# Kernel tuning notes

Hardware: AMD Instinct MI355X
Metric: run time of the kernel (lower is better)

The kernel has to match this reference:

```python
import jax, jax.numpy as jnp
import numpy as np

# 8-bit signed symmetric quantization grid (bit buffer in the module is set to 8 at runtime)
SAT_MAX = 127.0
SAT_MIN = -127.0


def _squant_stage(rn, re, un, ue, up_p, dn, de, dn_p):
    """One SQuant flip stage over the last axis (vectorized SQuant_func).

    For each row: e = sum(rounding_error); flip round(|e|) elements.
    If e < 0 (under-rounded overall) flip the highest-up-priority elements up,
    else flip the highest-down-priority elements down. The boundary (last,
    lowest-priority flipped) element gets a nonzero priority in the opposite
    direction so the next (coarser) stage can revert it — this reproduces the
    in-place priority update SQuant_func performs after zeroing priorities.
    All tensors have shape [..., K].
    """
    e_sum = jnp.sum(re, axis=-1)                                   # [...]
    n_flip = jnp.round(jnp.abs(e_sum)).astype(jnp.int32)[..., None]  # [...,1]
    flip_up = (e_sum < 0)[..., None]                               # [...,1]
    prio = jnp.where(flip_up, up_p, dn_p)
    order = jnp.argsort(-prio, axis=-1)        # descending priority
    rank = jnp.argsort(order, axis=-1)         # rank[i] = position of i in order
    mask = rank < n_flip                       # elements to flip
    rn2 = jnp.where(mask, jnp.where(flip_up, un, dn), rn)
    re2 = jnp.where(mask, jnp.where(flip_up, ue, de), re)
    # boundary element (rank == n_flip-1) gets opposite-direction priority
    boundary = mask & (rank == (n_flip - 1))
    b_prio = jnp.where(boundary, jnp.abs(re2), 0.0)
    up_p2 = jnp.where(flip_up, jnp.zeros_like(b_prio), b_prio)
    dn_p2 = jnp.where(flip_up, b_prio, jnp.zeros_like(b_prio))
    return rn2, re2, up_p2, dn_p2


def adaptive_round(x, t_min, t_max):
    rn = jnp.round(x)
    re = rn - x
    # up candidates: elements rounded down (re < 0) and not saturated high
    ue = jnp.where((x >= t_max) | (re > 0), 0.0, re)
    up_p = jnp.abs(ue)
    nz_u = ue != 0
    ue = jnp.where(nz_u, ue + 1.0, ue)
    un = jnp.where(nz_u, rn + 1.0, rn)
    # down candidates: elements rounded up (re > 0) and not saturated low
    de = jnp.where((x <= t_min) | (re < 0), 0.0, re)
    dn_p = jnp.abs(de)
    nz_d = de != 0
    de = jnp.where(nz_d, de - 1.0, de)
    dn = jnp.where(nz_d, rn - 1.0, rn)

    OC, IC = x.shape[0], x.shape[1]
    K = x.size // (OC * IC)
    shp_k = (OC, IC, K)         # squant-k: per (oc, ic) kernel row
    rn_k, re_k, up_p_k, dn_p_k = _squant_stage(
        rn.reshape(shp_k), re.reshape(shp_k),
        un.reshape(shp_k), ue.reshape(shp_k), up_p.reshape(shp_k),
        dn.reshape(shp_k), de.reshape(shp_k), dn_p.reshape(shp_k))
    shp_c = (1, OC, IC * K)     # squant-c: per oc channel row
    rn_c, _, _, _ = _squant_stage(
        rn_k.reshape(shp_c), re_k.reshape(shp_c),
        un.reshape(shp_c), ue.reshape(shp_c), up_p_k.reshape(shp_c),
        dn.reshape(shp_c), de.reshape(shp_c), dn_p_k.reshape(shp_c))
    return rn_c.reshape(x.shape)


def setup_inputs() -> dict:
    key = jax.random.key(0)
    tensor = jax.random.normal(key, (1024, 1024, 3, 3), dtype=jnp.float32)
    return {"tensor": tensor}


def reference(tensor) -> jnp.ndarray:
    # symmetric linear quantization params from tensor min/max (weight path)
    max_abs = jnp.maximum(jnp.abs(jnp.max(tensor)), jnp.abs(jnp.min(tensor)))
    scale = max_abs / SAT_MAX                       # element scale
    q = jnp.clip(tensor / scale, SAT_MIN, SAT_MAX)  # linear_quantize
    q = adaptive_round(q, SAT_MIN, SAT_MAX)         # SQuant adaptive rounding
    return q * scale                                # linear_dequantize
```

## Files before the change

### kernel.cpp

```cpp
#include <hip/hip_runtime.h>

#define OC 1024
#define ICN 1024
#define KK 9
#define NELEM (OC * ICN * KK)
#define CH (ICN * KK)
#define CH4 (CH / 4)
#define BT 512
#define KMB 1024

__global__ void __launch_bounds__(256) kmax_part(const float* __restrict__ x,
                                                 float* __restrict__ part) {
    __shared__ float s_m[4];
    const int tid = blockIdx.x * 256 + threadIdx.x;
    const int stride = KMB * 256;
    const float4* x4 = (const float4*)x;
    float m = 0.f;
    #pragma unroll
    for (int k = 0; k < 9; ++k) {
        float4 v = x4[tid + k * stride];
        m = fmaxf(m, fmaxf(fmaxf(fabsf(v.x), fabsf(v.y)), fmaxf(fabsf(v.z), fabsf(v.w))));
    }
    #pragma unroll
    for (int off = 32; off > 0; off >>= 1)
        m = fmaxf(m, __shfl_xor(m, off, 64));
    if ((threadIdx.x & 63) == 0) s_m[threadIdx.x >> 6] = m;
    __syncthreads();
    if (threadIdx.x == 0)
        part[blockIdx.x] = fmaxf(fmaxf(s_m[0], s_m[1]), fmaxf(s_m[2], s_m[3]));
}

__global__ void __launch_bounds__(256) kmax_atomic(const float* __restrict__ x,
                                                   unsigned* __restrict__ ws) {
    __shared__ float s_m[4];
    const int tid = blockIdx.x * 256 + threadIdx.x;
    const int stride = KMB * 256;
    const float4* x4 = (const float4*)x;
    float m = 0.f;
    #pragma unroll
    for (int k = 0; k < 9; ++k) {
        float4 v = x4[tid + k * stride];
        m = fmaxf(m, fmaxf(fmaxf(fabsf(v.x), fabsf(v.y)), fmaxf(fabsf(v.z), fabsf(v.w))));
    }
    #pragma unroll
    for (int off = 32; off > 0; off >>= 1)
        m = fmaxf(m, __shfl_xor(m, off, 64));
    if ((threadIdx.x & 63) == 0) s_m[threadIdx.x >> 6] = m;
    __syncthreads();
    if (threadIdx.x == 0) {
        m = fmaxf(fmaxf(s_m[0], s_m[1]), fmaxf(s_m[2], s_m[3]));
        atomicMax(ws, __float_as_uint(m));
    }
}

template <int C>
__device__ __forceinline__ void red_step(unsigned& key, unsigned& row) {
    unsigned k2 = (unsigned)__builtin_amdgcn_update_dpp(0, (int)key, C, 0xF, 0xF, false);
    unsigned r2 = (unsigned)__builtin_amdgcn_update_dpp(0, (int)row, C, 0xF, 0xF, false);
    if (k2 >= key) { key = k2; row = r2; }
}

__device__ __forceinline__ void wave_argmax(unsigned& key, unsigned& row) {
    red_step<0x111>(key, row);
    red_step<0x112>(key, row);
    red_step<0x114>(key, row);
    red_step<0x118>(key, row);
    red_step<0x142>(key, row);
    red_step<0x143>(key, row);
}

__global__ void __launch_bounds__(BT, 8) squant_kernel(const float* __restrict__ x,
                                                       float* __restrict__ out,
                                                       const float* __restrict__ part,
                                                       int nparts) {
    __shared__ __align__(16) signed char s_q[CH];
    __shared__ float s_res[ICN];
    __shared__ float s_prio[ICN];
    __shared__ int   s_meta[ICN];

    const int oc = blockIdx.x;
    const int t  = threadIdx.x;
    const long long ocbase = (long long)oc * CH;

    const float* p0 = x + ocbase + (long long)t * KK;
    const float* p1 = p0 + (long long)BT * KK;
    float a0[KK], a1[KK];
    #pragma unroll
    for (int k = 0; k < KK; ++k) a0[k] = p0[k];
    #pragma unroll
    for (int k = 0; k < KK; ++k) a1[k] = p1[k];

    float m;
    if (nparts > 0) {
        m = 0.f;
        #pragma unroll
        for (int i = 0; i < 16; ++i) m = fmaxf(m, part[(t & 63) + i * 64]);
        #pragma unroll
        for (int off = 32; off > 0; off >>= 1)
            m = fmaxf(m, __shfl_xor(m, off, 64));
    } else {
        m = __uint_as_float(((const unsigned*)part)[0]);
    }
    const float scale = m / 127.0f;
    const float iscale = 1.0f / scale;

    #pragma unroll
    for (int half = 0; half < 2; ++half) {
        const int row = t + half * BT;
        float rn[KK], re[KK];
        float e = 0.f;
        #pragma unroll
        for (int k = 0; k < KK; ++k) {
            float q = (half ? a1[k] : a0[k]) * iscale;
            q = fminf(fmaxf(q, -127.f), 127.f);
            float r = rintf(q);
            rn[k] = r;
            re[k] = r - q;
            e += re[k];
        }
        int nf = (int)rintf(fabsf(e));
        bool up = e < 0.f;
        unsigned flipped = 0u;
        int bidx = -1;
        float b_re = 0.f;
        for (int f = 0; f < nf; ++f) {
            float bp = 0.f; int bk = -1; float cre = 0.f;
            #pragma unroll
            for (int k = 0; k < KK; ++k) {
                bool cand = up ? (re[k] < 0.f) : (re[k] > 0.f);
                float p = (cand && !((flipped >> k) & 1u)) ? fabsf(re[k]) : 0.f;
                if (p > bp) { bp = p; bk = k; cre = re[k]; }
            }
            if (bk < 0) break;
            flipped |= (1u << bk);
            bidx = bk; b_re = cre;
        }
        int cnt = __popc(flipped);
        float sgn = up ? 1.f : -1.f;

        #pragma unroll
        for (int k = 0; k < KK; ++k) {
            float v = rn[k] + (((flipped >> k) & 1u) ? sgn : 0.f);
            s_q[row * KK + k] = (signed char)(int)v;
        }
        s_res[row] = e + sgn * (float)cnt;
        if (bidx >= 0) {
            s_prio[row] = fabsf(b_re + sgn);
            s_meta[row] = (row * KK + bidx) | ((up ? 1 : 0) << 16);
        } else {
            s_prio[row] = 0.f;
            s_meta[row] = 0;
        }
    }
    __syncthreads();

    if (t < 64) {
        float s = 0.f;
        #pragma unroll
        for (int i = 0; i < ICN / 64; ++i) s += s_res[t + i * 64];
        #pragma unroll
        for (int off = 32; off > 0; off >>= 1) s += __shfl_xor(s, off, 64);

        int n2 = (int)rintf(fabsf(s));
        bool up2 = s < 0.f;
        if (n2 > 0) {
            unsigned k[ICN / 64];
            #pragma unroll
            for (int i = 0; i < ICN / 64; ++i) {
                int r = t + i * 64;
                float pr = s_prio[r];
                int dir = s_meta[r] >> 16;
                bool match = ((dir != 0) != up2);
                unsigned bits = __float_as_uint(pr);
                k[i] = (pr > 0.f && match)
                         ? (((bits - 0x3F000000u + 1u) << 4) | (15u - (unsigned)i))
                         : 0u;
            }
            unsigned bk = 0u;
            #pragma unroll
            for (int i = 0; i < ICN / 64; ++i) bk = (k[i] > bk) ? k[i] : bk;
            unsigned brow = (unsigned)(t + (15 - (int)(bk & 15u)) * 64);

            unsigned fmask = 0u;
            int f = 0;
            for (; f < n2; ++f) {
                unsigned key = bk, row = brow;
                wave_argmax(key, row);
                unsigned kw = (unsigned)__builtin_amdgcn_readlane((int)key, 63);
                unsigned rw = (unsigned)__builtin_amdgcn_readlane((int)row, 63);
                if (kw == 0u) break;
                int iw = 15 - (int)(kw & 15u);
                bool owner = (t == (int)(rw & 63u));
                if (owner) fmask |= (1u << iw);
                unsigned zm = owner ? (1u << iw) : 0u;
                unsigned nb = 0u;
                #pragma unroll
                for (int i = 0; i < ICN / 64; ++i) {
                    unsigned ki = ((zm >> i) & 1u) ? 0u : k[i];
                    k[i] = ki;
                    nb = (ki > nb) ? ki : nb;
                }
                bk = nb;
                brow = (unsigned)(t + (15 - (int)(bk & 15u)) * 64);
            }

            #pragma unroll
            for (int i = 0; i < ICN / 64; ++i) {
                if ((fmask >> i) & 1u) {
                    int meta = s_meta[t + i * 64];
                    int gid = meta & 0xFFFF;
                    s_q[gid] = (signed char)(s_q[gid] + ((meta >> 16) ? -1 : 1));
                }
            }

            if (f < n2) {
                int remaining = n2 - f;
                if (remaining > CH) remaining = CH;
                for (int j = t; j < remaining; j += 64) {
                    float q = x[ocbase + j] * iscale;
                    q = fminf(fmaxf(q, -127.f), 127.f);
                    float r = rintf(q);
                    float rr = r - q;
                    float v = up2 ? ((rr < 0.f) ? r + 1.f : r)
                                  : ((rr > 0.f) ? r - 1.f : r);
                    s_q[j] = (signed char)(int)v;
                }
            }
        }
    }
    __syncthreads();

    const int* qw = (const int*)s_q;
    float4* o4 = (float4*)(out + ocbase);
    for (int i = t; i < CH4; i += BT) {
        int w = qw[i];
        float4 o;
        o.x = (float)((int)(signed char)(w        & 0xFF)) * scale;
        o.y = (float)((int)(signed char)((w >> 8)  & 0xFF)) * scale;
        o.z = (float)((int)(signed char)((w >> 16) & 0xFF)) * scale;
        o.w = (float)((int)(signed char)((w >> 24) & 0xFF)) * scale;
        o4[i] = o;
    }
}

extern "C" void kernel_launch(void* const* d_in, const int* in_sizes, int n_in,
                              void* d_out, int out_size, void* d_ws, size_t ws_size,
                              hipStream_t stream) {
    const float* x = (const float*)d_in[0];
    float* out = (float*)d_out;
    if (ws_size >= KMB * sizeof(float)) {
        float* part = (float*)d_ws;
        kmax_part<<<KMB, 256, 0, stream>>>(x, part);
        squant_kernel<<<OC, BT, 0, stream>>>(x, out, part, KMB);
    } else {
        unsigned* wsmax = (unsigned*)d_ws;
        hipMemsetAsync(d_ws, 0, 4, stream);
        kmax_atomic<<<KMB, 256, 0, stream>>>(x, wsmax);
        squant_kernel<<<OC, BT, 0, stream>>>(x, out, (const float*)d_ws, 0);
    }
}
```

Measured before the change: 104.2 us.

## Replace iterative wave argmax flip selection with radix threshold select

Replaces the loop that runs one DPP wave argmax per flipped element (n2 iterations) in the channel stage with a bitwise radix search for the n-th largest priority key. The search uses 28 wave-sum count passes, then selects every element above the threshold and fills the remaining slots from ties using a ballot rank. This bounds the serial work when many flips are needed, but it always pays the 28 reductions even when n2 is small. Because keys embed a unique row index, ties should be unique, so results should match.

```diff
diff --git a/kernel.cpp b/kernel.cpp
--- a/kernel.cpp
+++ b/kernel.cpp
@@ -54,19 +54,18 @@
 }
 
 template <int C>
-__device__ __forceinline__ void red_step(unsigned& key, unsigned& row) {
-    unsigned k2 = (unsigned)__builtin_amdgcn_update_dpp(0, (int)key, C, 0xF, 0xF, false);
-    unsigned r2 = (unsigned)__builtin_amdgcn_update_dpp(0, (int)row, C, 0xF, 0xF, false);
-    if (k2 >= key) { key = k2; row = r2; }
-}
-
-__device__ __forceinline__ void wave_argmax(unsigned& key, unsigned& row) {
-    red_step<0x111>(key, row);
-    red_step<0x112>(key, row);
-    red_step<0x114>(key, row);
-    red_step<0x118>(key, row);
-    red_step<0x142>(key, row);
-    red_step<0x143>(key, row);
+__device__ __forceinline__ unsigned dpp_add_step(unsigned v) {
+    unsigned o = (unsigned)__builtin_amdgcn_update_dpp(0, (int)v, C, 0xF, 0xF, false);
+    return v + o;
+}
+__device__ __forceinline__ unsigned wave_sum_u32(unsigned v) {
+    v = dpp_add_step<0x111>(v);
+    v = dpp_add_step<0x112>(v);
+    v = dpp_add_step<0x114>(v);
+    v = dpp_add_step<0x118>(v);
+    v = dpp_add_step<0x142>(v);
+    v = dpp_add_step<0x143>(v);
+    return (unsigned)__builtin_amdgcn_readlane((int)v, 63);
 }
 
 __global__ void __launch_bounds__(BT, 8) squant_kernel(const float* __restrict__ x,
@@ -176,40 +175,52 @@
                          ? (((bits - 0x3F000000u + 1u) << 4) | (15u - (unsigned)i))
                          : 0u;
             }
-            unsigned bk = 0u;
+
+            unsigned cloc = 0u;
             #pragma unroll
-            for (int i = 0; i < ICN / 64; ++i) bk = (k[i] > bk) ? k[i] : bk;
-            unsigned brow = (unsigned)(t + (15 - (int)(bk & 15u)) * 64);
-
-            unsigned fmask = 0u;
+            for (int i = 0; i < ICN / 64; ++i) cloc += (k[i] != 0u) ? 1u : 0u;
+            unsigned Ctot = wave_sum_u32(cloc);
+
             int f = 0;
-            for (; f < n2; ++f) {
-                unsigned key = bk, row = brow;
-                wave_argmax(key, row);
-                unsigned kw = (unsigned)__builtin_amdgcn_readlane((int)key, 63);
-                unsigned rw = (unsigned)__builtin_amdgcn_readlane((int)row, 63);
-                if (kw == 0u) break;
-                int iw = 15 - (int)(kw & 15u);
-                bool owner = (t == (int)(rw & 63u));
-                if (owner) fmask |= (1u << iw);
-                unsigned zm = owner ? (1u << iw) : 0u;
-                unsigned nb = 0u;
+            if (Ctot > 0u) {
+                unsigned nsel = ((unsigned)n2 < Ctot) ? (unsigned)n2 : Ctot;
+
+                unsigned T = 0u;
+                for (int b = 27; b >= 0; --b) {
+                    unsigned cand = T | (1u << b);
+                    unsigned c = 0u;
+                    #pragma unroll
+                    for (int i = 0; i < ICN / 64; ++i) c += (k[i] >= cand) ? 1u : 0u;
+                    if (wave_sum_u32(c) >= nsel) T = cand;
+                }
+
+                unsigned c1loc = 0u;
+                unsigned fmask = 0u;
                 #pragma unroll
                 for (int i = 0; i < ICN / 64; ++i) {
-                    unsigned ki = ((zm >> i) & 1u) ? 0u : k[i];
-                    k[i] = ki;
-                    nb = (ki > nb) ? ki : nb;
-                }
-                bk = nb;
-                brow = (unsigned)(t + (15 - (int)(bk & 15u)) * 64);
-            }
-
-            #pragma unroll
-            for (int i = 0; i < ICN / 64; ++i) {
-                if ((fmask >> i) & 1u) {
-                    int meta = s_meta[t + i * 64];
-                    int gid = meta & 0xFFFF;
-                    s_q[gid] = (signed char)(s_q[gid] + ((meta >> 16) ? -1 : 1));
+                    if (k[i] > T) { fmask |= (1u << i); c1loc += 1u; }
+                }
+                unsigned C1 = wave_sum_u32(c1loc);
+                int need = (int)nsel - (int)C1;
+
+                int tie_i = -1;
+                #pragma unroll
+                for (int i = 0; i < ICN / 64; ++i) {
+                    if (k[i] == T) tie_i = i;
+                }
+                unsigned long long tmask = __ballot(tie_i >= 0);
+                int rank = __popcll(tmask & ((1ull << t) - 1ull));
+                if (tie_i >= 0 && rank < need) fmask |= (1u << tie_i);
+
+                f = (int)nsel;
+
+                #pragma unroll
+                for (int i = 0; i < ICN / 64; ++i) {
+                    if ((fmask >> i) & 1u) {
+                        int meta = s_meta[t + i * 64];
+                        int gid = meta & 0xFFFF;
+                        s_q[gid] = (signed char)(s_q[gid] + ((meta >> 16) ? -1 : 1));
+                    }
                 }
             }
 
```

Measured after the change: 104.2 us. Within noise of the previous version (-0.0%).
